# Optimization experiments

Measured on AMD Instinct MI355X. Metric: run time of the kernel, lower is better.

## Reference

```python
import jax, jax.numpy as jnp
import numpy as np

B = 8192
D = 1024
NUM_HEADS = 16
HEAD_DIM = D // NUM_HEADS  # 64; only used as the softmax scale


def setup_inputs() -> dict:
    key = jax.random.key(0)
    ks = jax.random.split(key, 7)
    s = 1.0 / np.sqrt(D)
    return {
        "x": jax.random.normal(ks[0], (B, D), dtype=jnp.float32),
        "Wq": jax.random.normal(ks[1], (D, D), dtype=jnp.float32) * s,
        "bq": jax.random.normal(ks[2], (D,), dtype=jnp.float32) * s,
        "Wk": jax.random.normal(ks[3], (D, D), dtype=jnp.float32) * s,
        "bk": jax.random.normal(ks[4], (D,), dtype=jnp.float32) * s,
        "Wv": jax.random.normal(ks[5], (D, D), dtype=jnp.float32) * s,
        "bv": jax.random.normal(ks[6], (D,), dtype=jnp.float32) * s,
    }


def reference(x, Wq, bq, Wk, bk, Wv, bv):
    # Faithful to the torch module: x is 2D [B, D]; attention is over the batch axis.
    # nn.Linear computes x @ W.T + b
    Q = x @ Wq.T + bq            # [B, D]
    K = x @ Wk.T + bk            # [B, D]
    V = x @ Wv.T + bv            # [B, D]
    scale = 1.0 / jnp.sqrt(jnp.float32(HEAD_DIM))
    energy = (Q @ K.T) * scale   # [B, B]
    attn = jax.nn.softmax(energy, axis=-1)
    out = attn @ V               # [B, D]
    # torch: x.permute(0,1).contiguous().view(B, seq_len, -1) -> [B, D, 1]
    return out.reshape(B, D, 1)
```

## Files before the change

kernel.cpp:

```cpp
#include <hip/hip_runtime.h>
#include <hip/hip_bf16.h>

typedef _Float16 half_t;
typedef _Float16 f16x8 __attribute__((ext_vector_type(8)));
typedef _Float16 f16x4 __attribute__((ext_vector_type(4)));
typedef float f32x4 __attribute__((ext_vector_type(4)));

#define B_ROWS 8192
#define D_DIM  1024

__device__ __forceinline__ void gload_lds16(const void* g, void* l)
{
    __builtin_amdgcn_global_load_lds((const __attribute__((address_space(1))) void*)g,
                                     (__attribute__((address_space(3))) void*)l, 16, 0, 0);
}

__global__ __launch_bounds__(256)
void cvt_f32_f16(const float* __restrict__ in, half_t* __restrict__ out, int n)
{
    int i = (blockIdx.x * 256 + threadIdx.x) * 4;
    int stride = gridDim.x * 256 * 4;
    for (; i < n; i += stride) {
        float4 v = *(const float4*)&in[i];
        f16x4 o;
        o[0] = (half_t)v.x; o[1] = (half_t)v.y; o[2] = (half_t)v.z; o[3] = (half_t)v.w;
        *(f16x4*)&out[i] = o;
    }
}

__global__ __launch_bounds__(256)
void transpose_h(const half_t* __restrict__ in, half_t* __restrict__ out, int R, int C)
{
    __shared__ half_t t[64][65];
    int tilesC = C >> 6;
    int bc = blockIdx.x % tilesC;
    int br = blockIdx.x / tilesC;
    int r0 = br * 64, c0 = bc * 64;
    for (int e = threadIdx.x; e < 64 * 64; e += 256) {
        int r = e >> 6, c = e & 63;
        t[r][c] = in[(size_t)(r0 + r) * C + (c0 + c)];
    }
    __syncthreads();
    for (int e = threadIdx.x; e < 64 * 64; e += 256) {
        int r = e >> 6, c = e & 63;
        out[(size_t)(c0 + r) * R + (r0 + c)] = t[c][r];
    }
}

template<int EPI>
__device__ __forceinline__ void gemm8_core(
    const half_t* __restrict__ A, const half_t* __restrict__ Bm,
    const float* __restrict__ bias, void* __restrict__ Out,
    int lda, int ldb, int ldc, float scale,
    int row0, int col0, int ktile0, int nkt)
{
    __shared__ __align__(16) half_t As[4 * 8192];
    __shared__ __align__(16) half_t Bs[4 * 8192];

    const int tid  = threadIdx.x;
    const int lane = tid & 63;
    const int wid  = tid >> 6;
    const int wr   = wid >> 2;
    const int wcn  = wid & 3;
    const int l15  = lane & 15;
    const int l4   = lane >> 4;

    const int trow  = tid >> 3;
    const int tslot = (tid & 7) ^ (trow & 7);
    const char* Apan[2] = { (const char*)(A + (size_t)row0 * lda),
                            (const char*)(A + (size_t)(row0 + 128) * lda) };
    const char* Bpan[2] = { (const char*)(Bm + (size_t)col0 * ldb),
                            (const char*)(Bm + (size_t)(col0 + 128) * ldb) };
    const size_t aoff[2] = { (size_t)trow * lda * 2 + (size_t)tslot * 16,
                             (size_t)(trow + 64) * lda * 2 + (size_t)tslot * 16 };
    const size_t boff[2] = { (size_t)trow * ldb * 2 + (size_t)tslot * 16,
                             (size_t)(trow + 64) * ldb * 2 + (size_t)tslot * 16 };
    const int dstb[2] = { tid * 16, 8192 + tid * 16 };

    auto stageA = [&](int h, int s, int buf) {
        char* d = (char*)(As + (buf * 2 + h) * 8192);
        const char* g = Apan[h] + (size_t)(ktile0 + s) * 128;
        gload_lds16(g + aoff[0], d + dstb[0]);
        gload_lds16(g + aoff[1], d + dstb[1]);
    };
    auto stageB = [&](int h, int s, int buf) {
        char* d = (char*)(Bs + (buf * 2 + h) * 8192);
        const char* g = Bpan[h] + (size_t)(ktile0 + s) * 128;
        gload_lds16(g + boff[0], d + dstb[0]);
        gload_lds16(g + boff[1], d + dstb[1]);
    };
    auto rdA = [&](int mm, int kb, const half_t* base) -> f16x8 {
        int rih  = mm * 32 + wr * 16 + l15;
        int byte = rih * 128 + (((kb * 4 + l4) ^ (rih & 7)) << 4);
        return *(const f16x8*)((const char*)base + byte);
    };
    auto rdB = [&](int nn, int kb, const half_t* base) -> f16x8 {
        int rih  = nn * 64 + wcn * 16 + l15;
        int byte = rih * 128 + (((kb * 4 + l4) ^ (rih & 7)) << 4);
        return *(const f16x8*)((const char*)base + byte);
    };

    f32x4 acc[8][4] = {};
    f16x8 af[2][4], bf[2][2];

    {
        int s1 = (nkt > 1) ? 1 : 0;
        stageA(0, 0, 0); stageB(0, 0, 0); stageA(1, 0, 0); stageB(1, 0, 0);
        stageA(0, s1, 1); stageB(0, s1, 1);
    }
    asm volatile("s_waitcnt vmcnt(4)" ::: "memory");
    asm volatile("s_barrier" ::: "memory");

    for (int t = 0; t < nkt; ++t) {
        const int buf = t & 1;
        const half_t* A0 = As + (buf * 2 + 0) * 8192;
        const half_t* A1 = As + (buf * 2 + 1) * 8192;
        const half_t* B0 = Bs + (buf * 2 + 0) * 8192;
        const half_t* B1 = Bs + (buf * 2 + 1) * 8192;
        int t1  = t + 1; int t1s = (t1 < nkt) ? t1 : nkt - 1; int b1 = t1 & 1;
        int t2  = t + 2; int t2s = (t2 < nkt) ? t2 : nkt - 1;

        #pragma unroll
        for (int m = 0; m < 4; ++m) { af[0][m] = rdA(m, 0, A0); af[1][m] = rdA(m, 1, A0); }
        #pragma unroll
        for (int n = 0; n < 2; ++n) { bf[0][n] = rdB(n, 0, B0); bf[1][n] = rdB(n, 1, B0); }
        stageA(1, t1s, b1);
        asm volatile("s_barrier" ::: "memory");
        __builtin_amdgcn_s_setprio(1);
        #pragma unroll
        for (int kb = 0; kb < 2; ++kb)
            #pragma unroll
            for (int m = 0; m < 4; ++m)
                #pragma unroll
                for (int n = 0; n < 2; ++n)
                    acc[m][n] = __builtin_amdgcn_mfma_f32_16x16x32_f16(af[kb][m], bf[kb][n], acc[m][n], 0, 0, 0);
        __builtin_amdgcn_s_setprio(0);
        asm volatile("s_barrier" ::: "memory");

        #pragma unroll
        for (int n = 0; n < 2; ++n) { bf[0][n] = rdB(n, 0, B1); bf[1][n] = rdB(n, 1, B1); }
        stageB(1, t1s, b1);
        asm volatile("s_barrier" ::: "memory");
        __builtin_amdgcn_s_setprio(1);
        #pragma unroll
        for (int kb = 0; kb < 2; ++kb)
            #pragma unroll
            for (int m = 0; m < 4; ++m)
                #pragma unroll
                for (int n = 0; n < 2; ++n)
                    acc[m][n + 2] = __builtin_amdgcn_mfma_f32_16x16x32_f16(af[kb][m], bf[kb][n], acc[m][n + 2], 0, 0, 0);
        __builtin_amdgcn_s_setprio(0);
        asm volatile("s_barrier" ::: "memory");

        #pragma unroll
        for (int m = 0; m < 4; ++m) { af[0][m] = rdA(m, 0, A1); af[1][m] = rdA(m, 1, A1); }
        #pragma unroll
        for (int n = 0; n < 2; ++n) { bf[0][n] = rdB(n, 0, B0); bf[1][n] = rdB(n, 1, B0); }
        stageA(0, t2s, buf);
        asm volatile("s_barrier" ::: "memory");
        __builtin_amdgcn_s_setprio(1);
        #pragma unroll
        for (int kb = 0; kb < 2; ++kb)
            #pragma unroll
            for (int m = 0; m < 4; ++m)
                #pragma unroll
                for (int n = 0; n < 2; ++n)
                    acc[m + 4][n] = __builtin_amdgcn_mfma_f32_16x16x32_f16(af[kb][m], bf[kb][n], acc[m + 4][n], 0, 0, 0);
        __builtin_amdgcn_s_setprio(0);
        asm volatile("s_barrier" ::: "memory");

        #pragma unroll
        for (int n = 0; n < 2; ++n) { bf[0][n] = rdB(n, 0, B1); bf[1][n] = rdB(n, 1, B1); }
        stageB(0, t2s, buf);
        asm volatile("s_barrier" ::: "memory");
        __builtin_amdgcn_s_setprio(1);
        #pragma unroll
        for (int kb = 0; kb < 2; ++kb)
            #pragma unroll
            for (int m = 0; m < 4; ++m)
                #pragma unroll
                for (int n = 0; n < 2; ++n)
                    acc[m + 4][n + 2] = __builtin_amdgcn_mfma_f32_16x16x32_f16(af[kb][m], bf[kb][n], acc[m + 4][n + 2], 0, 0, 0);
        __builtin_amdgcn_s_setprio(0);
        asm volatile("s_waitcnt vmcnt(4)" ::: "memory");
        asm volatile("s_barrier" ::: "memory");
    }

    #pragma unroll
    for (int m = 0; m < 8; ++m) {
        int grow_base = row0 + m * 32 + wr * 16 + l4 * 4;
        #pragma unroll
        for (int n = 0; n < 4; ++n) {
            int gcol = col0 + n * 64 + wcn * 16 + l15;
            float badd = (EPI == 0) ? bias[gcol] : 0.0f;
            #pragma unroll
            for (int r = 0; r < 4; ++r) {
                float v = acc[m][n][r] * scale + badd;
                size_t idx = (size_t)(grow_base + r) * ldc + gcol;
                if (EPI == 2) ((float*)Out)[idx] = v;
                else          ((half_t*)Out)[idx] = (half_t)v;
            }
        }
    }
}

template<int EPI, int REMAP>
__global__ __launch_bounds__(512, 2)
void gemm8(const half_t* __restrict__ A, const half_t* __restrict__ Bm,
           const float* __restrict__ bias, void* __restrict__ Out,
           int lda, int ldb, int ldc, float scale, int nkt)
{
    int bx, by;
    if (REMAP) {
        int L = blockIdx.y * gridDim.x + blockIdx.x;
        int s = L >> 8;
        int u = L & 255;
        int xcd  = u & 7;
        int slot = u >> 3;
        by = (s >> 1) * 16 + xcd * 2 + (slot >> 4);
        bx = (s & 1) * 16 + (slot & 15);
    } else {
        int nwg = gridDim.x * gridDim.y;
        int bid = blockIdx.y * gridDim.x + blockIdx.x;
        if ((nwg & 7) == 0) { int c = nwg >> 3; bid = (bid & 7) * c + (bid >> 3); }
        bx = bid % gridDim.x; by = bid / gridDim.x;
    }
    gemm8_core<EPI>(A, Bm, bias, Out, lda, ldb, ldc, scale, by * 256, bx * 256, 0, nkt);
}

__global__ __launch_bounds__(512, 2)
void gemm8_qkv(const half_t* __restrict__ xh,
               const half_t* __restrict__ Wq, const half_t* __restrict__ Wk, const half_t* __restrict__ Wv,
               const float* __restrict__ bq, const float* __restrict__ bk, const float* __restrict__ bv,
               half_t* __restrict__ Q, half_t* __restrict__ K, half_t* __restrict__ V)
{
    int z = blockIdx.z;
    const half_t* W = (z == 0) ? Wq : (z == 1) ? Wk : Wv;
    const float*  b = (z == 0) ? bq : (z == 1) ? bk : bv;
    half_t*       O = (z == 0) ? Q  : (z == 1) ? K  : V;
    gemm8_core<0>(xh, W, b, O, D_DIM, D_DIM, D_DIM, 1.0f,
                  blockIdx.y * 256, blockIdx.x * 256, 0, D_DIM / 64);
}

__global__ __launch_bounds__(512, 2)
void gemm8_pv(const half_t* __restrict__ S, const half_t* __restrict__ Vt,
              float* __restrict__ part0, float* __restrict__ part1)
{
    int z = blockIdx.z;
    float* O = z ? part1 : part0;
    gemm8_core<2>(S, Vt, nullptr, O, B_ROWS, B_ROWS, D_DIM, 1.0f,
                  blockIdx.y * 256, blockIdx.x * 256, z * (B_ROWS / 128), B_ROWS / 128);
}

__global__ __launch_bounds__(256)
void add_f32(const float* __restrict__ a, float* __restrict__ out, int n)
{
    int i = (blockIdx.x * 256 + threadIdx.x) * 4;
    int stride = gridDim.x * 256 * 4;
    for (; i < n; i += stride) {
        float4 x = *(const float4*)&out[i];
        float4 y = *(const float4*)&a[i];
        x.x += y.x; x.y += y.y; x.z += y.z; x.w += y.w;
        *(float4*)&out[i] = x;
    }
}

__global__ __launch_bounds__(256)
void softmax_rows(half_t* __restrict__ S, int ncol)
{
    const int row = blockIdx.x;
    half_t* srow = S + (size_t)row * ncol;
    const int tid = threadIdx.x;

    float ev[32];
    float m = -1e30f;
    #pragma unroll
    for (int it = 0; it < 4; ++it) {
        int j = it * 2048 + tid * 8;
        f16x8 v = *(const f16x8*)&srow[j];
        #pragma unroll
        for (int t = 0; t < 8; ++t) {
            float f = (float)v[t];
            ev[it * 8 + t] = f;
            m = fmaxf(m, f);
        }
    }
    #pragma unroll
    for (int o = 32; o; o >>= 1) m = fmaxf(m, __shfl_down(m, o));
    __shared__ float redm[8];
    __shared__ float reds[8];
    if ((tid & 63) == 0) redm[tid >> 6] = m;
    __syncthreads();
    m = fmaxf(fmaxf(redm[0], redm[1]), fmaxf(redm[2], redm[3]));

    float s = 0.0f;
    #pragma unroll
    for (int e = 0; e < 32; ++e) {
        float ex = __expf(ev[e] - m);
        ev[e] = ex;
        s += ex;
    }
    #pragma unroll
    for (int o = 32; o; o >>= 1) s += __shfl_down(s, o);
    if ((tid & 63) == 0) reds[tid >> 6] = s;
    __syncthreads();
    s = reds[0] + reds[1] + reds[2] + reds[3];
    float inv = 1.0f / s;

    #pragma unroll
    for (int it = 0; it < 4; ++it) {
        int j = it * 2048 + tid * 8;
        f16x8 o8;
        #pragma unroll
        for (int t = 0; t < 8; ++t) o8[t] = (half_t)(ev[it * 8 + t] * inv);
        *(f16x8*)&srow[j] = o8;
    }
}

extern "C" void kernel_launch(void* const* d_in, const int* in_sizes, int n_in,
                              void* d_out, int out_size, void* d_ws, size_t ws_size,
                              hipStream_t stream)
{
    const float* x  = (const float*)d_in[0];
    const float* Wq = (const float*)d_in[1];
    const float* bq = (const float*)d_in[2];
    const float* Wk = (const float*)d_in[3];
    const float* bk = (const float*)d_in[4];
    const float* Wv = (const float*)d_in[5];
    const float* bv = (const float*)d_in[6];
    float* out = (float*)d_out;

    const int Bb = B_ROWS, Dd = D_DIM;

    char* w = (char*)d_ws;
    size_t off = 0;
    auto carve = [&](size_t bytes) {
        void* p = w + off;
        off += (bytes + 255) & ~(size_t)255;
        return p;
    };
    half_t* xh  = (half_t*)carve((size_t)Bb * Dd * 2);
    half_t* Wqh = (half_t*)carve((size_t)Dd * Dd * 2);
    half_t* Wkh = (half_t*)carve((size_t)Dd * Dd * 2);
    half_t* Wvh = (half_t*)carve((size_t)Dd * Dd * 2);
    half_t* Qh  = (half_t*)carve((size_t)Bb * Dd * 2);
    half_t* Kh  = (half_t*)carve((size_t)Bb * Dd * 2);
    half_t* Vh  = (half_t*)carve((size_t)Bb * Dd * 2);
    half_t* S   = (half_t*)carve((size_t)Bb * Bb * 2);
    half_t* Vt  = xh;
    float*  part1 = (float*)Qh;

    cvt_f32_f16<<<2048, 256, 0, stream>>>(x,  xh,  Bb * Dd);
    cvt_f32_f16<<<1024, 256, 0, stream>>>(Wq, Wqh, Dd * Dd);
    cvt_f32_f16<<<1024, 256, 0, stream>>>(Wk, Wkh, Dd * Dd);
    cvt_f32_f16<<<1024, 256, 0, stream>>>(Wv, Wvh, Dd * Dd);

    dim3 gqkv(Dd / 256, Bb / 256, 3);
    gemm8_qkv<<<gqkv, 512, 0, stream>>>(xh, Wqh, Wkh, Wvh, bq, bk, bv, Qh, Kh, Vh);

    transpose_h<<<(Dd / 64) * (Bb / 64), 256, 0, stream>>>(Vh, Vt, Bb, Dd);

    dim3 gs(Bb / 256, Bb / 256);
    gemm8<1, 1><<<gs, 512, 0, stream>>>(Qh, Kh, nullptr, S, Dd, Dd, Bb, 0.125f, Dd / 64);

    softmax_rows<<<Bb, 256, 0, stream>>>(S, Bb);

    dim3 gpv(Dd / 256, Bb / 256, 2);
    gemm8_pv<<<gpv, 512, 0, stream>>>(S, Vt, out, part1);
    add_f32<<<2048, 256, 0, stream>>>(part1, out, Bb * Dd);
}
```

Before: 434.6 us.

## Switch GEMM core to 32x32x16 MFMA and remap PV blocks across XCDs

Each warp's inner GEMM now issues 32x32x16 f16 MFMAs instead of 16x16x32 ones, with each warp owning a 64x32 sub-tile per quadrant. Fragment loads and the epilogue index math change to match, and the B fragments for the two column halves are kept in separate registers so they can be reused across phases. The intent is fewer LDS reads per flop and fewer MFMA issues. Separately, the PV kernel's block indices are remapped so consecutive blocks on the same XCD share rows and L2 locality. The new layout could raise register pressure, and the epilogue writes a strided row pattern.

```diff
diff --git a/kernel.cpp b/kernel.cpp
--- a/kernel.cpp
+++ b/kernel.cpp
@@ -5,6 +5,7 @@
 typedef _Float16 f16x8 __attribute__((ext_vector_type(8)));
 typedef _Float16 f16x4 __attribute__((ext_vector_type(4)));
 typedef float f32x4 __attribute__((ext_vector_type(4)));
+typedef float f32x16 __attribute__((ext_vector_type(16)));
 
 #define B_ROWS 8192
 #define D_DIM  1024
@@ -62,8 +63,8 @@
     const int wid  = tid >> 6;
     const int wr   = wid >> 2;
     const int wcn  = wid & 3;
-    const int l15  = lane & 15;
-    const int l4   = lane >> 4;
+    const int l31  = lane & 31;
+    const int l32  = lane >> 5;
 
     const int trow  = tid >> 3;
     const int tslot = (tid & 7) ^ (trow & 7);
@@ -89,19 +90,20 @@
         gload_lds16(g + boff[0], d + dstb[0]);
         gload_lds16(g + boff[1], d + dstb[1]);
     };
-    auto rdA = [&](int mm, int kb, const half_t* base) -> f16x8 {
-        int rih  = mm * 32 + wr * 16 + l15;
-        int byte = rih * 128 + (((kb * 4 + l4) ^ (rih & 7)) << 4);
+    auto rdA = [&](int mm, int kc, const half_t* base) -> f16x8 {
+        int rih  = wr * 64 + mm * 32 + l31;
+        int byte = rih * 128 + (((kc * 2 + l32) ^ (rih & 7)) << 4);
         return *(const f16x8*)((const char*)base + byte);
     };
-    auto rdB = [&](int nn, int kb, const half_t* base) -> f16x8 {
-        int rih  = nn * 64 + wcn * 16 + l15;
-        int byte = rih * 128 + (((kb * 4 + l4) ^ (rih & 7)) << 4);
+    auto rdB = [&](int kc, const half_t* base) -> f16x8 {
+        int rih  = wcn * 32 + l31;
+        int byte = rih * 128 + (((kc * 2 + l32) ^ (rih & 7)) << 4);
         return *(const f16x8*)((const char*)base + byte);
     };
 
-    f32x4 acc[8][4] = {};
-    f16x8 af[2][4], bf[2][2];
+    f32x16 acc[2][2][2] = {};
+    f16x8 af[2][4];
+    f16x8 bfP[4], bfQ[4];
 
     {
         int s1 = (nkt > 1) ? 1 : 0;
@@ -121,84 +123,80 @@
         int t2  = t + 2; int t2s = (t2 < nkt) ? t2 : nkt - 1;
 
         #pragma unroll
-        for (int m = 0; m < 4; ++m) { af[0][m] = rdA(m, 0, A0); af[1][m] = rdA(m, 1, A0); }
-        #pragma unroll
-        for (int n = 0; n < 2; ++n) { bf[0][n] = rdB(n, 0, B0); bf[1][n] = rdB(n, 1, B0); }
+        for (int mm = 0; mm < 2; ++mm)
+            #pragma unroll
+            for (int kc = 0; kc < 4; ++kc) af[mm][kc] = rdA(mm, kc, A0);
+        #pragma unroll
+        for (int kc = 0; kc < 4; ++kc) bfP[kc] = rdB(kc, B0);
         stageA(1, t1s, b1);
         asm volatile("s_barrier" ::: "memory");
         __builtin_amdgcn_s_setprio(1);
         #pragma unroll
-        for (int kb = 0; kb < 2; ++kb)
-            #pragma unroll
-            for (int m = 0; m < 4; ++m)
-                #pragma unroll
-                for (int n = 0; n < 2; ++n)
-                    acc[m][n] = __builtin_amdgcn_mfma_f32_16x16x32_f16(af[kb][m], bf[kb][n], acc[m][n], 0, 0, 0);
+        for (int kc = 0; kc < 4; ++kc)
+            #pragma unroll
+            for (int mm = 0; mm < 2; ++mm)
+                acc[0][mm][0] = __builtin_amdgcn_mfma_f32_32x32x16_f16(af[mm][kc], bfP[kc], acc[0][mm][0], 0, 0, 0);
         __builtin_amdgcn_s_setprio(0);
         asm volatile("s_barrier" ::: "memory");
 
         #pragma unroll
-        for (int n = 0; n < 2; ++n) { bf[0][n] = rdB(n, 0, B1); bf[1][n] = rdB(n, 1, B1); }
+        for (int kc = 0; kc < 4; ++kc) bfQ[kc] = rdB(kc, B1);
         stageB(1, t1s, b1);
         asm volatile("s_barrier" ::: "memory");
         __builtin_amdgcn_s_setprio(1);
         #pragma unroll
-        for (int kb = 0; kb < 2; ++kb)
-            #pragma unroll
-            for (int m = 0; m < 4; ++m)
-                #pragma unroll
-                for (int n = 0; n < 2; ++n)
-                    acc[m][n + 2] = __builtin_amdgcn_mfma_f32_16x16x32_f16(af[kb][m], bf[kb][n], acc[m][n + 2], 0, 0, 0);
+        for (int kc = 0; kc < 4; ++kc)
+            #pragma unroll
+            for (int mm = 0; mm < 2; ++mm)
+                acc[0][mm][1] = __builtin_amdgcn_mfma_f32_32x32x16_f16(af[mm][kc], bfQ[kc], acc[0][mm][1], 0, 0, 0);
         __builtin_amdgcn_s_setprio(0);
         asm volatile("s_barrier" ::: "memory");
 
         #pragma unroll
-        for (int m = 0; m < 4; ++m) { af[0][m] = rdA(m, 0, A1); af[1][m] = rdA(m, 1, A1); }
-        #pragma unroll
-        for (int n = 0; n < 2; ++n) { bf[0][n] = rdB(n, 0, B0); bf[1][n] = rdB(n, 1, B0); }
+        for (int mm = 0; mm < 2; ++mm)
+            #pragma unroll
+            for (int kc = 0; kc < 4; ++kc) af[mm][kc] = rdA(mm, kc, A1);
         stageA(0, t2s, buf);
         asm volatile("s_barrier" ::: "memory");
         __builtin_amdgcn_s_setprio(1);
         #pragma unroll
-        for (int kb = 0; kb < 2; ++kb)
-            #pragma unroll
-            for (int m = 0; m < 4; ++m)
-                #pragma unroll
-                for (int n = 0; n < 2; ++n)
-                    acc[m + 4][n] = __builtin_amdgcn_mfma_f32_16x16x32_f16(af[kb][m], bf[kb][n], acc[m + 4][n], 0, 0, 0);
+        for (int kc = 0; kc < 4; ++kc)
+            #pragma unroll
+            for (int mm = 0; mm < 2; ++mm)
+                acc[1][mm][0] = __builtin_amdgcn_mfma_f32_32x32x16_f16(af[mm][kc], bfP[kc], acc[1][mm][0], 0, 0, 0);
         __builtin_amdgcn_s_setprio(0);
         asm volatile("s_barrier" ::: "memory");
 
-        #pragma unroll
-        for (int n = 0; n < 2; ++n) { bf[0][n] = rdB(n, 0, B1); bf[1][n] = rdB(n, 1, B1); }
         stageB(0, t2s, buf);
         asm volatile("s_barrier" ::: "memory");
         __builtin_amdgcn_s_setprio(1);
         #pragma unroll
-        for (int kb = 0; kb < 2; ++kb)
-            #pragma unroll
-            for (int m = 0; m < 4; ++m)
-                #pragma unroll
-                for (int n = 0; n < 2; ++n)
-                    acc[m + 4][n + 2] = __builtin_amdgcn_mfma_f32_16x16x32_f16(af[kb][m], bf[kb][n], acc[m + 4][n + 2], 0, 0, 0);
+        for (int kc = 0; kc < 4; ++kc)
+            #pragma unroll
+            for (int mm = 0; mm < 2; ++mm)
+                acc[1][mm][1] = __builtin_amdgcn_mfma_f32_32x32x16_f16(af[mm][kc], bfQ[kc], acc[1][mm][1], 0, 0, 0);
         __builtin_amdgcn_s_setprio(0);
         asm volatile("s_waitcnt vmcnt(4)" ::: "memory");
         asm volatile("s_barrier" ::: "memory");
     }
 
     #pragma unroll
-    for (int m = 0; m < 8; ++m) {
-        int grow_base = row0 + m * 32 + wr * 16 + l4 * 4;
-        #pragma unroll
-        for (int n = 0; n < 4; ++n) {
-            int gcol = col0 + n * 64 + wcn * 16 + l15;
-            float badd = (EPI == 0) ? bias[gcol] : 0.0f;
-            #pragma unroll
-            for (int r = 0; r < 4; ++r) {
-                float v = acc[m][n][r] * scale + badd;
-                size_t idx = (size_t)(grow_base + r) * ldc + gcol;
-                if (EPI == 2) ((float*)Out)[idx] = v;
-                else          ((half_t*)Out)[idx] = (half_t)v;
+    for (int h = 0; h < 2; ++h) {
+        #pragma unroll
+        for (int mm = 0; mm < 2; ++mm) {
+            int r0 = row0 + h * 128 + wr * 64 + mm * 32 + 4 * l32;
+            #pragma unroll
+            for (int nh = 0; nh < 2; ++nh) {
+                int gcol = col0 + nh * 128 + wcn * 32 + l31;
+                float badd = (EPI == 0) ? bias[gcol] : 0.0f;
+                #pragma unroll
+                for (int g = 0; g < 16; ++g) {
+                    int row = r0 + (g & 3) + 8 * (g >> 2);
+                    float v = acc[h][mm][nh][g] * scale + badd;
+                    size_t idx = (size_t)row * ldc + gcol;
+                    if (EPI == 2) ((float*)Out)[idx] = v;
+                    else          ((half_t*)Out)[idx] = (half_t)v;
+                }
             }
         }
     }
@@ -246,10 +244,15 @@
 void gemm8_pv(const half_t* __restrict__ S, const half_t* __restrict__ Vt,
               float* __restrict__ part0, float* __restrict__ part1)
 {
-    int z = blockIdx.z;
+    int h = blockIdx.z * 128 + blockIdx.y * 4 + blockIdx.x;
+    int l = (h & 7) * 32 + (h >> 3);
+    int z  = l >> 7;
+    int r  = l & 127;
+    int by = r >> 2;
+    int bx = r & 3;
     float* O = z ? part1 : part0;
     gemm8_core<2>(S, Vt, nullptr, O, B_ROWS, B_ROWS, D_DIM, 1.0f,
-                  blockIdx.y * 256, blockIdx.x * 256, z * (B_ROWS / 128), B_ROWS / 128);
+                  by * 256, bx * 256, z * (B_ROWS / 128), B_ROWS / 128);
 }
 
 __global__ __launch_bounds__(256)
```

New measurement: 438.4 us. No clear change (+0.9%).
